# Performance work log

Measured on AMD Instinct MI355X. Metric: run time of the kernel, lower is better.

The kernel has to match this reference:

```python
import jax, jax.numpy as jnp
import numpy as np

B, S, D = 1, 2048, 4096
H, KV, HD = 32, 8, 128
C = 4096  # cache length
THETA = 1000000.0
NEG = -1e9


def setup_inputs() -> dict:
    key = jax.random.key(0)
    ks = jax.random.split(key, 8)
    std = 0.02
    x = jax.random.normal(ks[0], (B, S, D), jnp.float32)
    wq = jax.random.normal(ks[1], (H * HD, D), jnp.float32) * std
    wk = jax.random.normal(ks[2], (KV * HD, D), jnp.float32) * std
    wv = jax.random.normal(ks[3], (KV * HD, D), jnp.float32) * std
    wo = jax.random.normal(ks[4], (D, H * HD), jnp.float32) * std
    k_cache = jnp.zeros((B, KV, C, HD), jnp.float32)
    v_cache = jnp.zeros((B, KV, C, HD), jnp.float32)
    # rotary tables (real/imag of freqs_cis)
    inv_freq = 1.0 / (THETA ** (jnp.arange(0, HD, 2, dtype=jnp.float32) / HD))  # [HD/2]
    t = jnp.arange(C, dtype=jnp.float32)
    freqs = jnp.outer(t, inv_freq)  # [C, HD/2]
    cos, sin = jnp.cos(freqs), jnp.sin(freqs)
    # causal additive mask over cache positions
    mask = jnp.where(jnp.tril(jnp.ones((C, C), bool)), 0.0, NEG).astype(jnp.float32)
    storage_idx = jnp.arange(S, dtype=jnp.int32)
    return {"x": x, "wq": wq, "wk": wk, "wv": wv, "wo": wo,
            "k_cache": k_cache, "v_cache": v_cache,
            "cos": cos, "sin": sin, "mask": mask, "storage_idx": storage_idx}


def _rope(x, cos, sin):
    # x: [B, h, S, HD]; cos/sin: [S, HD/2] -> complex mult on interleaved pairs
    xr, xi = x[..., 0::2], x[..., 1::2]
    c = cos[None, None, :, :]
    s = sin[None, None, :, :]
    or_, oi_ = xr * c - xi * s, xr * s + xi * c
    return jnp.stack([or_, oi_], axis=-1).reshape(x.shape)


def reference(x, wq, wk, wv, wo, k_cache, v_cache, cos, sin, mask, storage_idx):
    bsz, seqlen, _ = x.shape
    xq = jnp.einsum('bsd,ed->bse', x, wq).reshape(bsz, seqlen, H, HD).transpose(0, 2, 1, 3)
    xk = jnp.einsum('bsd,ed->bse', x, wk).reshape(bsz, seqlen, KV, HD).transpose(0, 2, 1, 3)
    xv = jnp.einsum('bsd,ed->bse', x, wv).reshape(bsz, seqlen, KV, HD).transpose(0, 2, 1, 3)
    cos_g, sin_g = cos[storage_idx], sin[storage_idx]
    xq = _rope(xq, cos_g, sin_g)
    xk = _rope(xk, cos_g, sin_g)
    # scatter into KV cache at storage_idx along the position axis
    keys = k_cache.at[:, :, storage_idx, :].set(xk)
    values = v_cache.at[:, :, storage_idx, :].set(xv)
    # GQA: repeat kv heads (kv-head-major, matches expand+reshape)
    rep = H // KV
    keys = jnp.repeat(keys, rep, axis=1)      # [B, H, C, HD]
    values = jnp.repeat(values, rep, axis=1)  # [B, H, C, HD]
    scores = jnp.einsum('bhqd,bhkd->bhqk', xq, keys) / np.sqrt(HD)
    scores = scores + mask[storage_idx][None, None, :, :]
    attn = jax.nn.softmax(scores, axis=-1)
    out = jnp.einsum('bhqk,bhkd->bhqd', attn, values)
    out = out.transpose(0, 2, 1, 3).reshape(bsz, seqlen, H * HD)
    return jnp.einsum('bse,de->bsd', out, wo)
```

## Files before the change

### kernel.cpp

```cpp
#include <hip/hip_runtime.h>
#include <cstdint>
#include <cstddef>

#define S_LEN 2048
#define DM    4096
#define NH    32
#define NKV   8
#define HDIM  128
#define EQ    4096
#define EKV   1024
#define SC_LOG2E 0.1275325477889277f

typedef unsigned short u16;
typedef short bf16x8 __attribute__((ext_vector_type(8)));
typedef float f32x4  __attribute__((ext_vector_type(4)));

__device__ __forceinline__ u16 f2bf(float f) {
  union { float f; unsigned u; } v; v.f = f;
  unsigned r = v.u + 0x7FFFu + ((v.u >> 16) & 1u);
  return (u16)(r >> 16);
}
__device__ __forceinline__ float bf2f(u16 b) {
  union { unsigned u; float f; } v; v.u = ((unsigned)b) << 16;
  return v.f;
}
__device__ __forceinline__ void glds16(const void* g, void* l) {
  __builtin_amdgcn_global_load_lds((const __attribute__((address_space(1))) void*)g,
                                   (__attribute__((address_space(3))) void*)l, 16, 0, 0);
}

__global__ void cast_all(const float* __restrict__ x, const float* __restrict__ wq,
                         const float* __restrict__ wk, const float* __restrict__ wv,
                         const float* __restrict__ wo,
                         u16* __restrict__ xb, u16* __restrict__ wqb,
                         u16* __restrict__ wkb, u16* __restrict__ wvb,
                         u16* __restrict__ wob) {
  const size_t stride = (size_t)gridDim.x * blockDim.x;
  for (size_t u = (size_t)blockIdx.x * blockDim.x + threadIdx.x; u < 12582912u; u += stride) {
    const float* in; u16* outp; size_t i;
    if (u < 2097152u)      { in = x;  outp = xb;  i = u; }
    else if (u < 6291456u) { in = wq; outp = wqb; i = u - 2097152u; }
    else if (u < 7340032u) { in = wk; outp = wkb; i = u - 6291456u; }
    else if (u < 8388608u) { in = wv; outp = wvb; i = u - 7340032u; }
    else                   { in = wo; outp = wob; i = u - 8388608u; }
    float4 f = ((const float4*)in)[i];
    ushort4 b;
    b.x = f2bf(f.x); b.y = f2bf(f.y); b.z = f2bf(f.z); b.w = f2bf(f.w);
    ((ushort4*)outp)[i] = b;
  }
}

template<int UN>
__device__ __forceinline__ void stage_t(const u16* __restrict__ g, int ldg, int k0,
                                        u16* ldsp, int t) {
  const int wb = t & ~63;
#pragma unroll
  for (int j = 0; j < UN / 256; ++j) {
    const int U = j * 256 + t;
    const int row = U >> 3, u = U & 7;
    const int uu = u ^ (row & 7);
    glds16(g + (size_t)row * ldg + k0 + uu * 8, ldsp + (size_t)(j * 256 + wb) * 8);
  }
}

template<int NF, bool QKV3>
__global__ __launch_bounds__(256, 2)
void gemm2p(const u16* __restrict__ A, const u16* __restrict__ B,
            void* __restrict__ Cq, u16* __restrict__ Ck, u16* __restrict__ Cv,
            int K) {
  constexpr int BN = 64 * NF;
  constexpr int AT = 128 * 64;
  constexpr int BT = BN * 64;
  __shared__ u16 lds[2 * (AT + BT)];
  const int t = threadIdx.x;
  const int l = t & 63, lr = l & 15, lg = l >> 4;
  const int wid = t >> 6, wm = wid >> 1, wn = wid & 1;

  const int bid = blockIdx.x;
  const int xcd = bid & 7, j = bid >> 3;
  const int bx = xcd * 4 + (j >> 4);
  const int by = j & 15;
  const int m0 = by * 128, n0 = bx * BN;
  const int KT = K >> 6;

  const u16* Ab = A + (size_t)m0 * K;
  const u16* Bb = B + (size_t)n0 * K;

  f32x4 acc[4][2 * NF] = {};

  stage_t<1024>(Ab, K, 0, &lds[0], t);
  stage_t<BT / 8>(Bb, K, 0, &lds[2 * AT], t);
  __syncthreads();

  int cur = 0;
#pragma unroll 1
  for (int tau = 0; tau < KT; ++tau) {
    const int kn = (tau + 1 < KT ? tau + 1 : KT - 1) * 64;
    stage_t<1024>(Ab, K, kn, &lds[(cur ^ 1) * AT], t);
    stage_t<BT / 8>(Bb, K, kn, &lds[2 * AT + (cur ^ 1) * BT], t);

    const int aBase = cur * AT;
    const int bBase = 2 * AT + cur * BT;

    bf16x8 af[4][2];
#pragma unroll
    for (int mf = 0; mf < 4; ++mf)
#pragma unroll
      for (int kk = 0; kk < 2; ++kk) {
        const int row = wm * 64 + mf * 16 + lr;
        const int uu = ((kk * 4 + lg) ^ (row & 7)) * 8;
        af[mf][kk] = *(const bf16x8*)&lds[aBase + row * 64 + uu];
      }

#pragma unroll
    for (int n = 0; n < 2 * NF; ++n) {
      const int brow = wn * (32 * NF) + n * 16 + lr;
      const int u0 = ((0 * 4 + lg) ^ (brow & 7)) * 8;
      const int u1 = ((1 * 4 + lg) ^ (brow & 7)) * 8;
      bf16x8 b0 = *(const bf16x8*)&lds[bBase + brow * 64 + u0];
      bf16x8 b1 = *(const bf16x8*)&lds[bBase + brow * 64 + u1];
#pragma unroll
      for (int mf = 0; mf < 4; ++mf) {
        acc[mf][n] = __builtin_amdgcn_mfma_f32_16x16x32_bf16(af[mf][0], b0, acc[mf][n], 0, 0, 0);
        acc[mf][n] = __builtin_amdgcn_mfma_f32_16x16x32_bf16(af[mf][1], b1, acc[mf][n], 0, 0, 0);
      }
    }
    __syncthreads();
    cur ^= 1;
  }

#pragma unroll
  for (int mf = 0; mf < 4; ++mf) {
    const int row = m0 + wm * 64 + mf * 16 + lg * 4;
#pragma unroll
    for (int n = 0; n < 2 * NF; ++n) {
      const int gc = n0 + wn * (32 * NF) + n * 16 + lr;
#pragma unroll
      for (int r = 0; r < 4; ++r) {
        if constexpr (QKV3) {
          if (gc < 4096)
            ((u16*)Cq)[(size_t)(row + r) * 4096 + gc] = f2bf(acc[mf][n][r]);
          else if (gc < 5120)
            Ck[(size_t)(row + r) * 1024 + (gc - 4096)] = f2bf(acc[mf][n][r]);
          else
            Cv[(size_t)(row + r) * 1024 + (gc - 5120)] = f2bf(acc[mf][n][r]);
        } else {
          ((float*)Cq)[(size_t)(row + r) * 4096 + gc] = acc[mf][n][r];
        }
      }
    }
  }
}

__global__ void rope_all(u16* __restrict__ qd, u16* __restrict__ kd,
                         const float* __restrict__ cosb, const float* __restrict__ sinb,
                         const int* __restrict__ sidx) {
  const int u = blockIdx.x * blockDim.x + threadIdx.x;
  u16* base; int s, b;
  if (u < 1048576) {
    base = qd + (size_t)u * 8;
    s = u >> 9;
    b = u & 15;
  } else if (u < 1310720) {
    const int u2 = u - 1048576;
    base = kd + (size_t)u2 * 8;
    s = u2 >> 7;
    b = u2 & 15;
  } else return;
  const int pos = sidx[s];
  const float4 c  = *(const float4*)&cosb[pos * 64 + b * 4];
  const float4 sn = *(const float4*)&sinb[pos * 64 + b * 4];
  uint4 raw = *(uint4*)base;
  u16* pe = (u16*)&raw;
  const float cc[4] = {c.x, c.y, c.z, c.w};
  const float ss[4] = {sn.x, sn.y, sn.z, sn.w};
#pragma unroll
  for (int j = 0; j < 4; ++j) {
    const float xr = bf2f(pe[2 * j]), xi = bf2f(pe[2 * j + 1]);
    pe[2 * j]     = f2bf(xr * cc[j] - xi * ss[j]);
    pe[2 * j + 1] = f2bf(xr * ss[j] + xi * cc[j]);
  }
  *(uint4*)base = raw;
}

__global__ void transpose_v(const u16* __restrict__ v, u16* __restrict__ vt) {
  __shared__ u16 tile[32][33];
  const int tx = threadIdx.x, ty = threadIdx.y;
  const int c0 = blockIdx.x * 32, s0 = blockIdx.y * 32;
#pragma unroll
  for (int j = 0; j < 32; j += 8)
    tile[ty + j][tx] = v[(size_t)(s0 + ty + j) * EKV + c0 + tx];
  __syncthreads();
#pragma unroll
  for (int j = 0; j < 32; j += 8)
    vt[(size_t)(c0 + ty + j) * S_LEN + s0 + tx] = tile[tx][ty + j];
}

#define ATTN_STAGE(TK, BUF) { \
  const int kv0s = (TK) * 64; \
  _Pragma("unroll") \
  for (int hh = 0; hh < 4; ++hh) { \
    const int f = hh * 256 + t; \
    { const int row = f >> 4, uu = f & 15, us = uu ^ (row & 7); \
      glds16(&k[(size_t)(kv0s + row) * EKV + kvh * HDIM + us * 8], &lK[BUF][(hh * 256 + wb) * 8]); } \
    { const int row = f >> 3, uu = f & 7, us = uu ^ (row & 7); \
      glds16(&vt[(size_t)(kvh * HDIM + row) * S_LEN + kv0s + us * 8], &lV[BUF][(hh * 256 + wb) * 8]); } \
  } }

__global__ __launch_bounds__(256, 2)
void attn_fwd(const u16* __restrict__ q, const u16* __restrict__ k,
              const u16* __restrict__ vt, u16* __restrict__ ao) {
  __shared__ u16 lK[2][64 * 128];
  __shared__ u16 lV[2][128 * 64];
  __shared__ u16 lP[4 * 16 * 72];
  const int t = threadIdx.x, w = t >> 6, l = t & 63;
  const int lr = l & 15, lg = l >> 4;
  const int wb = t & ~63;
  const int p = blockIdx.x, h = blockIdx.y;
  const int kvh = h >> 2;
  u16* lPw = &lP[w * (16 * 72)];

#pragma unroll 1
  for (int ph = 0; ph < 2; ++ph) {
    const int qt = ph ? (31 - p) : p;
    const int q0 = qt * 64 + w * 16;
    const int nt = qt + 1;

    bf16x8 qa[4];
#pragma unroll
    for (int kc = 0; kc < 4; ++kc)
      qa[kc] = *(const bf16x8*)&q[(size_t)(q0 + lr) * EQ + h * HDIM + kc * 32 + lg * 8];

    f32x4 o[8] = {};
    float mrun[4], lrun[4];
#pragma unroll
    for (int r = 0; r < 4; ++r) { mrun[r] = -1e30f; lrun[r] = 0.f; }

    int cur = 0;
    ATTN_STAGE(0, 0);
    __syncthreads();

#pragma unroll 1
    for (int tk = 0; tk < nt; ++tk) {
      const int kv0 = tk * 64;
      if (tk + 1 < nt) ATTN_STAGE(tk + 1, cur ^ 1);
      const u16* lKc = lK[cur];
      const u16* lVc = lV[cur];

      f32x4 sc[4] = {};
#pragma unroll
      for (int n = 0; n < 4; ++n) {
#pragma unroll
        for (int kc = 0; kc < 4; ++kc) {
          const int row = n * 16 + lr;
          const int us = (kc * 4 + lg) ^ (row & 7);
          bf16x8 bk = *(const bf16x8*)&lKc[row * 128 + us * 8];
          sc[n] = __builtin_amdgcn_mfma_f32_16x16x32_bf16(qa[kc], bk, sc[n], 0, 0, 0);
        }
      }

#pragma unroll
      for (int n = 0; n < 4; ++n) {
        const int kvc = kv0 + n * 16 + lr;
#pragma unroll
        for (int r = 0; r < 4; ++r) {
          const int qr = q0 + lg * 4 + r;
          const float v = sc[n][r] * SC_LOG2E;
          sc[n][r] = (kvc > qr) ? -1e30f : v;
        }
      }
#pragma unroll
      for (int r = 0; r < 4; ++r) {
        float v = fmaxf(fmaxf(sc[0][r], sc[1][r]), fmaxf(sc[2][r], sc[3][r]));
        v = fmaxf(v, __shfl_xor(v, 1));
        v = fmaxf(v, __shfl_xor(v, 2));
        v = fmaxf(v, __shfl_xor(v, 4));
        v = fmaxf(v, __shfl_xor(v, 8));
        const float mn = fmaxf(mrun[r], v);
        const float sf = __builtin_amdgcn_exp2f(mrun[r] - mn);
        mrun[r] = mn;
        float rs = 0.f;
#pragma unroll
        for (int n = 0; n < 4; ++n) {
          const float pv = __builtin_amdgcn_exp2f(sc[n][r] - mn);
          sc[n][r] = pv;
          rs += pv;
        }
        rs += __shfl_xor(rs, 1);
        rs += __shfl_xor(rs, 2);
        rs += __shfl_xor(rs, 4);
        rs += __shfl_xor(rs, 8);
        lrun[r] = lrun[r] * sf + rs;
#pragma unroll
        for (int nh = 0; nh < 8; ++nh) o[nh][r] *= sf;
      }
#pragma unroll
      for (int n = 0; n < 4; ++n)
#pragma unroll
        for (int r = 0; r < 4; ++r)
          lPw[(lg * 4 + r) * 72 + n * 16 + lr] = f2bf(sc[n][r]);

#pragma unroll
      for (int kc2 = 0; kc2 < 2; ++kc2) {
        bf16x8 pa = *(const bf16x8*)&lPw[lr * 72 + kc2 * 32 + lg * 8];
#pragma unroll
        for (int nh = 0; nh < 8; ++nh) {
          const int row = nh * 16 + lr;
          const int us = (kc2 * 4 + lg) ^ (row & 7);
          bf16x8 bv = *(const bf16x8*)&lVc[row * 64 + us * 8];
          o[nh] = __builtin_amdgcn_mfma_f32_16x16x32_bf16(pa, bv, o[nh], 0, 0, 0);
        }
      }
      __syncthreads();
      cur ^= 1;
    }

#pragma unroll
    for (int nh = 0; nh < 8; ++nh)
#pragma unroll
      for (int r = 0; r < 4; ++r) {
        const float val = o[nh][r] / lrun[r];
        ao[(size_t)(q0 + lg * 4 + r) * EQ + h * HDIM + nh * 16 + lr] = f2bf(val);
      }
  }
}

extern "C" void kernel_launch(void* const* d_in, const int* in_sizes, int n_in,
                              void* d_out, int out_size, void* d_ws, size_t ws_size,
                              hipStream_t stream) {
  (void)in_sizes; (void)n_in; (void)out_size; (void)ws_size;
  const float* x    = (const float*)d_in[0];
  const float* wq   = (const float*)d_in[1];
  const float* wk   = (const float*)d_in[2];
  const float* wv   = (const float*)d_in[3];
  const float* wo   = (const float*)d_in[4];
  const float* cosb = (const float*)d_in[7];
  const float* sinb = (const float*)d_in[8];
  const int*   sidx = (const int*)d_in[10];
  float* out = (float*)d_out;

  u16* ws  = (u16*)d_ws;
  u16* xb  = ws;
  u16* wqb = xb  + (size_t)S_LEN * DM;
  u16* wkb = wqb + (size_t)EQ * DM;
  u16* wvb = wkb + (size_t)EKV * DM;
  u16* wob = wvb + (size_t)EKV * DM;
  u16* qb  = wob + (size_t)DM * EQ;
  u16* kb  = qb  + (size_t)S_LEN * EQ;
  u16* vb  = kb  + (size_t)S_LEN * EKV;
  u16* vtb = vb  + (size_t)S_LEN * EKV;
  u16* aob = vtb + (size_t)S_LEN * EKV;

  cast_all<<<2048, 256, 0, stream>>>(x, wq, wk, wv, wo, xb, wqb, wkb, wvb, wob);
  gemm2p<3, true><<<512, 256, 0, stream>>>(xb, wqb, qb, kb, vb, DM);
  rope_all<<<5120, 256, 0, stream>>>(qb, kb, cosb, sinb, sidx);
  transpose_v<<<dim3(EKV / 32, S_LEN / 32), dim3(32, 8), 0, stream>>>(vb, vtb);
  attn_fwd<<<dim3(16, NH), 256, 0, stream>>>(qb, kb, vtb, aob);
  gemm2p<2, false><<<512, 256, 0, stream>>>(aob, wob, out, nullptr, nullptr, EQ);
}
```

Baseline: 321.6 us.

## Single-buffer attention K/V tiles for higher occupancy and merge rope with V transpose

The attention kernel drops its double-buffered LDS K/V staging for a single buffer, reloaded each tile between two barriers, and raises launch bounds from 2 to 3 blocks per CU. The aim is more resident waves to hide latency in place of software prefetch overlap. The RoPE and V-transpose kernels are also fused into one launch via block-index dispatch, removing a kernel launch. The risk is that load latency is now exposed, since global-to-LDS copies no longer overlap with MFMA work within a block.

```diff
diff --git a/kernel.cpp b/kernel.cpp
--- a/kernel.cpp
+++ b/kernel.cpp
@@ -152,66 +152,69 @@
   }
 }
 
-__global__ void rope_all(u16* __restrict__ qd, u16* __restrict__ kd,
-                         const float* __restrict__ cosb, const float* __restrict__ sinb,
-                         const int* __restrict__ sidx) {
-  const int u = blockIdx.x * blockDim.x + threadIdx.x;
-  u16* base; int s, b;
-  if (u < 1048576) {
-    base = qd + (size_t)u * 8;
-    s = u >> 9;
-    b = u & 15;
-  } else if (u < 1310720) {
-    const int u2 = u - 1048576;
-    base = kd + (size_t)u2 * 8;
-    s = u2 >> 7;
-    b = u2 & 15;
-  } else return;
-  const int pos = sidx[s];
-  const float4 c  = *(const float4*)&cosb[pos * 64 + b * 4];
-  const float4 sn = *(const float4*)&sinb[pos * 64 + b * 4];
-  uint4 raw = *(uint4*)base;
-  u16* pe = (u16*)&raw;
-  const float cc[4] = {c.x, c.y, c.z, c.w};
-  const float ss[4] = {sn.x, sn.y, sn.z, sn.w};
-#pragma unroll
-  for (int j = 0; j < 4; ++j) {
-    const float xr = bf2f(pe[2 * j]), xi = bf2f(pe[2 * j + 1]);
-    pe[2 * j]     = f2bf(xr * cc[j] - xi * ss[j]);
-    pe[2 * j + 1] = f2bf(xr * ss[j] + xi * cc[j]);
-  }
-  *(uint4*)base = raw;
-}
-
-__global__ void transpose_v(const u16* __restrict__ v, u16* __restrict__ vt) {
-  __shared__ u16 tile[32][33];
-  const int tx = threadIdx.x, ty = threadIdx.y;
-  const int c0 = blockIdx.x * 32, s0 = blockIdx.y * 32;
-#pragma unroll
-  for (int j = 0; j < 32; j += 8)
-    tile[ty + j][tx] = v[(size_t)(s0 + ty + j) * EKV + c0 + tx];
-  __syncthreads();
-#pragma unroll
-  for (int j = 0; j < 32; j += 8)
-    vt[(size_t)(c0 + ty + j) * S_LEN + s0 + tx] = tile[tx][ty + j];
-}
-
-#define ATTN_STAGE(TK, BUF) { \
+__global__ void rope_tr(u16* __restrict__ qd, u16* __restrict__ kd,
+                        const float* __restrict__ cosb, const float* __restrict__ sinb,
+                        const int* __restrict__ sidx,
+                        const u16* __restrict__ v, u16* __restrict__ vt) {
+  const int bid = blockIdx.x, t = threadIdx.x;
+  if (bid < 5120) {
+    const int u = bid * 256 + t;
+    u16* base; int s, b;
+    if (u < 1048576) {
+      base = qd + (size_t)u * 8;
+      s = u >> 9;
+      b = u & 15;
+    } else {
+      const int u2 = u - 1048576;
+      base = kd + (size_t)u2 * 8;
+      s = u2 >> 7;
+      b = u2 & 15;
+    }
+    const int pos = sidx[s];
+    const float4 c  = *(const float4*)&cosb[pos * 64 + b * 4];
+    const float4 sn = *(const float4*)&sinb[pos * 64 + b * 4];
+    uint4 raw = *(uint4*)base;
+    u16* pe = (u16*)&raw;
+    const float cc[4] = {c.x, c.y, c.z, c.w};
+    const float ss[4] = {sn.x, sn.y, sn.z, sn.w};
+#pragma unroll
+    for (int j = 0; j < 4; ++j) {
+      const float xr = bf2f(pe[2 * j]), xi = bf2f(pe[2 * j + 1]);
+      pe[2 * j]     = f2bf(xr * cc[j] - xi * ss[j]);
+      pe[2 * j + 1] = f2bf(xr * ss[j] + xi * cc[j]);
+    }
+    *(uint4*)base = raw;
+  } else {
+    __shared__ u16 tile[32][33];
+    const int tb = bid - 5120;
+    const int c0 = (tb & 31) * 32, s0 = (tb >> 5) * 32;
+    const int tx = t & 31, ty = t >> 5;
+#pragma unroll
+    for (int j = 0; j < 32; j += 8)
+      tile[ty + j][tx] = v[(size_t)(s0 + ty + j) * EKV + c0 + tx];
+    __syncthreads();
+#pragma unroll
+    for (int j = 0; j < 32; j += 8)
+      vt[(size_t)(c0 + ty + j) * S_LEN + s0 + tx] = tile[tx][ty + j];
+  }
+}
+
+#define ATTN_STAGE(TK) { \
   const int kv0s = (TK) * 64; \
   _Pragma("unroll") \
   for (int hh = 0; hh < 4; ++hh) { \
     const int f = hh * 256 + t; \
     { const int row = f >> 4, uu = f & 15, us = uu ^ (row & 7); \
-      glds16(&k[(size_t)(kv0s + row) * EKV + kvh * HDIM + us * 8], &lK[BUF][(hh * 256 + wb) * 8]); } \
+      glds16(&k[(size_t)(kv0s + row) * EKV + kvh * HDIM + us * 8], &lK[(hh * 256 + wb) * 8]); } \
     { const int row = f >> 3, uu = f & 7, us = uu ^ (row & 7); \
-      glds16(&vt[(size_t)(kvh * HDIM + row) * S_LEN + kv0s + us * 8], &lV[BUF][(hh * 256 + wb) * 8]); } \
+      glds16(&vt[(size_t)(kvh * HDIM + row) * S_LEN + kv0s + us * 8], &lV[(hh * 256 + wb) * 8]); } \
   } }
 
-__global__ __launch_bounds__(256, 2)
+__global__ __launch_bounds__(256, 3)
 void attn_fwd(const u16* __restrict__ q, const u16* __restrict__ k,
               const u16* __restrict__ vt, u16* __restrict__ ao) {
-  __shared__ u16 lK[2][64 * 128];
-  __shared__ u16 lV[2][128 * 64];
+  __shared__ u16 lK[64 * 128];
+  __shared__ u16 lV[128 * 64];
   __shared__ u16 lP[4 * 16 * 72];
   const int t = threadIdx.x, w = t >> 6, l = t & 63;
   const int lr = l & 15, lg = l >> 4;
@@ -236,16 +239,12 @@
 #pragma unroll
     for (int r = 0; r < 4; ++r) { mrun[r] = -1e30f; lrun[r] = 0.f; }
 
-    int cur = 0;
-    ATTN_STAGE(0, 0);
-    __syncthreads();
-
 #pragma unroll 1
     for (int tk = 0; tk < nt; ++tk) {
       const int kv0 = tk * 64;
-      if (tk + 1 < nt) ATTN_STAGE(tk + 1, cur ^ 1);
-      const u16* lKc = lK[cur];
-      const u16* lVc = lV[cur];
+      __syncthreads();
+      ATTN_STAGE(tk);
+      __syncthreads();
 
       f32x4 sc[4] = {};
 #pragma unroll
@@ -254,7 +253,7 @@
         for (int kc = 0; kc < 4; ++kc) {
           const int row = n * 16 + lr;
           const int us = (kc * 4 + lg) ^ (row & 7);
-          bf16x8 bk = *(const bf16x8*)&lKc[row * 128 + us * 8];
+          bf16x8 bk = *(const bf16x8*)&lK[row * 128 + us * 8];
           sc[n] = __builtin_amdgcn_mfma_f32_16x16x32_bf16(qa[kc], bk, sc[n], 0, 0, 0);
         }
       }
@@ -307,12 +306,10 @@
         for (int nh = 0; nh < 8; ++nh) {
           const int row = nh * 16 + lr;
           const int us = (kc2 * 4 + lg) ^ (row & 7);
-          bf16x8 bv = *(const bf16x8*)&lVc[row * 64 + us * 8];
+          bf16x8 bv = *(const bf16x8*)&lV[row * 64 + us * 8];
           o[nh] = __builtin_amdgcn_mfma_f32_16x16x32_bf16(pa, bv, o[nh], 0, 0, 0);
         }
       }
-      __syncthreads();
-      cur ^= 1;
     }
 
 #pragma unroll
@@ -353,8 +350,7 @@
 
   cast_all<<<2048, 256, 0, stream>>>(x, wq, wk, wv, wo, xb, wqb, wkb, wvb, wob);
   gemm2p<3, true><<<512, 256, 0, stream>>>(xb, wqb, qb, kb, vb, DM);
-  rope_all<<<5120, 256, 0, stream>>>(qb, kb, cosb, sinb, sidx);
-  transpose_v<<<dim3(EKV / 32, S_LEN / 32), dim3(32, 8), 0, stream>>>(vb, vtb);
+  rope_tr<<<7168, 256, 0, stream>>>(qb, kb, cosb, sinb, sidx, vb, vtb);
   attn_fwd<<<dim3(16, NH), 256, 0, stream>>>(qb, kb, vtb, aob);
   gemm2p<2, false><<<512, 256, 0, stream>>>(aob, wob, out, nullptr, nullptr, EQ);
 }
```

Result: no change. 319.4 us (-0.7%).
